# Optimization experiments

Hardware: AMD Instinct MI355X
Metric: run time of the kernel (lower is better)

## Reference

```python
import jax, jax.numpy as jnp
import numpy as np

EMBED_DIM = 1024
HID = EMBED_DIM // 2
N = 32768
L2_REG = 0.001
BN_EPS = 1e-5


def setup_inputs() -> dict:
    key = jax.random.key(0)
    ks = jax.random.split(key, 8)
    inp = {
        "item_emb": jax.random.normal(ks[0], (N, EMBED_DIM), jnp.float32),
        "pos_item_emb": jax.random.normal(ks[1], (N, EMBED_DIM), jnp.float32),
        "neg_item_emb": jax.random.normal(ks[2], (N, EMBED_DIM), jnp.float32),
        # Linear 1: embed_dim -> embed_dim/2 (xavier_normal init, zero bias)
        "W1": jax.random.normal(ks[3], (HID, EMBED_DIM), jnp.float32) * np.sqrt(2.0 / (EMBED_DIM + HID)),
        "b1": jnp.zeros((HID,), jnp.float32),
        # BatchNorm1d params / running stats (eval-mode semantics)
        "gamma": jnp.ones((HID,), jnp.float32),
        "beta": jnp.zeros((HID,), jnp.float32),
        "run_mean": jnp.zeros((HID,), jnp.float32),
        "run_var": jnp.ones((HID,), jnp.float32),
        # Linear 2: embed_dim/2 -> embed_dim
        "W2": jax.random.normal(ks[4], (EMBED_DIM, HID), jnp.float32) * np.sqrt(2.0 / (EMBED_DIM + HID)),
        "b2": jnp.zeros((EMBED_DIM,), jnp.float32),
    }
    return inp


def _net(x, W1, b1, gamma, beta, run_mean, run_var, W2, b2):
    # Linear -> BatchNorm1d (eval stats) -> LeakyReLU(0.1) -> (Dropout=identity) -> Linear
    h = x @ W1.T + b1                                   # [N, HID]
    h = (h - run_mean) * jax.lax.rsqrt(run_var + BN_EPS) * gamma + beta
    h = jnp.where(h >= 0, h, 0.1 * h)
    return h @ W2.T + b2                                # [N, EMBED_DIM]


def reference(item_emb, pos_item_emb, neg_item_emb,
              W1, b1, gamma, beta, run_mean, run_var, W2, b2):
    net = lambda x: _net(x, W1, b1, gamma, beta, run_mean, run_var, W2, b2)
    anchor_e = net(item_emb)
    pos_e = net(pos_item_emb)
    neg_e = net(neg_item_emb)

    dist_pos = jnp.linalg.norm(anchor_e - pos_e, axis=1)  # [N]
    dist_neg = jnp.linalg.norm(anchor_e - neg_e, axis=1)  # [N]

    # fused replacement of the per-sample python loop
    margins = jnp.where(dist_neg < dist_pos, dist_pos - dist_neg, 0.0)
    margin = jnp.quantile(margins, 0.25)  # Q1, linear interpolation (matches torch)

    loss_triplet = jax.nn.relu(dist_neg ** 2 - dist_pos ** 2 + margin)
    l2 = L2_REG * (jnp.sum(anchor_e ** 2) + jnp.sum(pos_e ** 2) + jnp.sum(neg_e ** 2)) / anchor_e.shape[0]
    return jnp.mean(loss_triplet + l2)
```

## Files before the change

### kernel.cpp

```cpp
#include <hip/hip_runtime.h>

#define NROWS 32768
#define DIM   1024
#define HIDD  512
#define M3    (3*NROWS)

using bf16x8 = __attribute__((ext_vector_type(8))) short;
using f32x4  = __attribute__((ext_vector_type(4))) float;

#define MFMA16(a,b,c) __builtin_amdgcn_mfma_f32_16x16x32_bf16(a,b,c,0,0,0)
#define WAIT_VM(N)  asm volatile("s_waitcnt vmcnt(" #N ")" ::: "memory")
#define WAIT_LGKM0  asm volatile("s_waitcnt lgkmcnt(0)" ::: "memory")
#define MEMFENCE    asm volatile("" ::: "memory")
#define BAR()       __builtin_amdgcn_s_barrier()
#define SCHEDB()    __builtin_amdgcn_sched_barrier(0)
#define SP1()       __builtin_amdgcn_s_setprio(1)
#define SP0()       __builtin_amdgcn_s_setprio(0)

static __device__ __forceinline__ unsigned short f2bf(float f) {
    unsigned u = __float_as_uint(f);
    u += 0x7FFFu + ((u >> 16) & 1u);
    return (unsigned short)(u >> 16);
}
static __device__ __forceinline__ unsigned cvtpk(float a, float b) {
    unsigned r;
    asm("v_cvt_pk_bf16_f32 %0, %1, %2" : "=v"(r) : "v"(a), "v"(b));
    return r;
}
static __device__ __forceinline__ void gload16(const void* gsrc, void* ldst) {
    __builtin_amdgcn_global_load_lds(
        (const __attribute__((address_space(1))) unsigned int*)gsrc,
        (__attribute__((address_space(3))) unsigned int*)ldst,
        16, 0, 0);
}

__global__ __launch_bounds__(256)
void cvt2_kernel(const float* __restrict__ src1, unsigned short* __restrict__ dst1,
                 const float* __restrict__ src2, unsigned short* __restrict__ dst2,
                 int n4each)
{
    const int i = blockIdx.x * 256 + threadIdx.x;
    const float* src = (i < n4each) ? src1 : src2;
    unsigned short* dst = (i < n4each) ? dst1 : dst2;
    const int j = (i < n4each) ? i : (i - n4each);
    if (j < n4each) {
        float4 v = reinterpret_cast<const float4*>(src)[j];
        uint2 o;
        o.x = cvtpk(v.x, v.y);
        o.y = cvtpk(v.z, v.w);
        reinterpret_cast<uint2*>(dst)[j] = o;
    }
}

__global__ __launch_bounds__(512)
void gemm1_mfma(const float* __restrict__ x0, const float* __restrict__ x1,
                const float* __restrict__ x2,
                const unsigned short* __restrict__ W1bf,
                const float* __restrict__ b1, const float* __restrict__ gamma,
                const float* __restrict__ beta, const float* __restrict__ rmean,
                const float* __restrict__ rvar,
                unsigned short* __restrict__ h)
{
    __shared__ unsigned short Abuf[128*64];
    __shared__ unsigned short Bbuf[2*128*32];

    const int lin = blockIdx.x;
    const int wgid = (lin & 7) * 384 + (lin >> 3);
    const int cb = wgid & 3;
    const int rb = wgid >> 2;
    const int tid  = threadIdx.x;
    const int lane = tid & 63, w = tid >> 6;
    const int wr = w >> 2, wc = w & 3;
    const int row0 = rb * 128;
    const int s = row0 >> 15;
    const float* x = (s == 0) ? x0 : (s == 1 ? x1 : x2);
    const int rl0 = row0 & (NROWS - 1);
    const int col0 = cb * 128;
    const int l15 = lane & 15, lq = lane >> 4;

    f32x4 acc[4][2] = {};
    float4 aR[4];

    #pragma unroll
    for (int p = 0; p < 4; ++p) {
        const int f = p * 512 + tid;
        const int r = f >> 4, c4 = f & 15;
        aR[p] = *reinterpret_cast<const float4*>(&x[(size_t)(rl0 + r) * DIM + c4 * 4]);
    }

    for (int t = 0; t < 16; ++t) {
        const int k0 = t * 64;
        #pragma unroll
        for (int p = 0; p < 4; ++p) {
            const int f = p * 512 + tid;
            const int r = f >> 4, c4 = f & 15;
            const unsigned off = (unsigned)((r * 128 + c4 * 8) ^ ((r & 7) << 4));
            uint2 o;
            o.x = cvtpk(aR[p].x, aR[p].y);
            o.y = cvtpk(aR[p].z, aR[p].w);
            *reinterpret_cast<uint2*>(reinterpret_cast<char*>(Abuf) + off) = o;
        }
        #pragma unroll
        for (int c = 0; c < 2; ++c) {
            const int f = c * 512 + tid;
            const int panel = f >> 9;
            const int cc = (f >> 2) & 127;
            const int chunk = (f & 3) ^ ((cc >> 1) & 3);
            gload16(&W1bf[(size_t)(col0 + cc) * DIM + k0 + panel * 32 + chunk * 8],
                    reinterpret_cast<char*>(Bbuf) + (size_t)f * 16);
        }
        __syncthreads();
        if (t < 15) {
            #pragma unroll
            for (int p = 0; p < 4; ++p) {
                const int f = p * 512 + tid;
                const int r = f >> 4, c4 = f & 15;
                aR[p] = *reinterpret_cast<const float4*>(
                    &x[(size_t)(rl0 + r) * DIM + k0 + 64 + c4 * 4]);
            }
        }
        bf16x8 bfv[2][2];
        #pragma unroll
        for (int kk = 0; kk < 2; ++kk)
            #pragma unroll
            for (int n = 0; n < 2; ++n) {
                const int colr = wc*32 + n*16 + l15;
                const int slq = lq ^ ((colr >> 1) & 3);
                bfv[kk][n] = *reinterpret_cast<const bf16x8*>(
                    reinterpret_cast<char*>(Bbuf) + kk*8192 + colr*64 + slq*16);
            }
        #pragma unroll
        for (int kk = 0; kk < 2; ++kk)
            #pragma unroll
            for (int m = 0; m < 4; ++m) {
                const int row = wr*64 + m*16 + l15;
                const unsigned ab = (unsigned)((row*128 + kk*64 + lq*16) ^ ((row & 7) << 4));
                bf16x8 af = *reinterpret_cast<const bf16x8*>(
                    reinterpret_cast<char*>(Abuf) + ab);
                #pragma unroll
                for (int n = 0; n < 2; ++n)
                    acc[m][n] = MFMA16(af, bfv[kk][n], acc[m][n]);
            }
        __syncthreads();
    }

    float As[2], Bsc[2];
    #pragma unroll
    for (int n = 0; n < 2; ++n) {
        const int c = col0 + wc*32 + n*16 + l15;
        const float inv = rsqrtf(rvar[c] + 1e-5f);
        As[n]  = inv * gamma[c];
        Bsc[n] = (b1[c] - rmean[c]) * As[n] + beta[c];
    }
    #pragma unroll
    for (int m = 0; m < 4; ++m) {
        const int rbase = row0 + wr*64 + m*16 + lq*4;
        #pragma unroll
        for (int n = 0; n < 2; ++n) {
            const int c = col0 + wc*32 + n*16 + l15;
            #pragma unroll
            for (int i = 0; i < 4; ++i) {
                float v = fmaf(acc[m][n][i], As[n], Bsc[n]);
                v = (v >= 0.f) ? v : 0.1f * v;
                h[(size_t)(rbase + i) * HIDD + c] = f2bf(v);
            }
        }
    }
}

__global__ __launch_bounds__(512, 1)
void gemm2_mfma(const unsigned short* __restrict__ h,
                const unsigned short* __restrict__ W2bf,
                const float* __restrict__ b2,
                float* __restrict__ pdp, float* __restrict__ pdn,
                float* __restrict__ pl2)
{
    __shared__ char smem[114688];
    char* const Ab = smem;
    char* const Bb = smem + 49152;

    const int lin = blockIdx.x;
    const int wgid = (lin & 7) * 256 + (lin >> 3);
    const int cb = wgid & 3;
    const int rb = wgid >> 2;
    const int tid  = threadIdx.x;
    const int lane = tid & 63, w = tid >> 6;
    const int wm = w >> 2, wn = w & 3;
    const int row0 = rb * 64;
    const int col0 = cb * 256;
    const int l15 = lane & 15, lq = lane >> 4;

    f32x4 acc[6][4] = {};

    auto issueA = [&](int k0, char* Adst) {
        #pragma unroll
        for (int i = 0; i < 3; ++i) {
            const int f = i * 512 + tid;
            const int mrow = f >> 3, c = f & 7;
            const int mf = mrow >> 4, rr = mrow & 15;
            const int ss = mf % 3, rf = mf / 3;
            gload16(&h[((size_t)ss * NROWS + row0 + rf * 16 + rr) * HIDD + k0 + ((c ^ (mrow & 7)) << 3)],
                    Adst + f * 16);
        }
    };
    auto issueB = [&](int k0, char* Bdst) {
        #pragma unroll
        for (int i = 0; i < 4; ++i) {
            const int f = i * 512 + tid;
            const int col = f >> 3, c = f & 7;
            gload16(&W2bf[(size_t)(col0 + col) * HIDD + k0 + ((c ^ (col & 7)) << 3)],
                    Bdst + f * 16);
        }
    };
    auto readA = [&](bf16x8 (&a)[3][2], int mh, char* Abase) {
        #pragma unroll
        for (int mm = 0; mm < 3; ++mm) {
            const int row = (wm * 6 + mh * 3 + mm) * 16 + l15;
            const int swz = (row & 7) << 4;
            #pragma unroll
            for (int ks = 0; ks < 2; ++ks)
                a[mm][ks] = *reinterpret_cast<const bf16x8*>(
                    Abase + ((row * 128 + ks * 64 + lq * 16) ^ swz));
        }
    };
    auto readB = [&](bf16x8 (&b)[2][2], int nh, char* Bbase) {
        #pragma unroll
        for (int nn = 0; nn < 2; ++nn) {
            const int col = wn * 64 + (nh * 2 + nn) * 16 + l15;
            const int swz = (col & 7) << 4;
            #pragma unroll
            for (int ks = 0; ks < 2; ++ks)
                b[nn][ks] = *reinterpret_cast<const bf16x8*>(
                    Bbase + ((col * 128 + ks * 64 + lq * 16) ^ swz));
        }
    };

    issueA(0, Ab);
    MEMFENCE;
    issueB(0, Bb);
    WAIT_VM(0);
    BAR();

    for (int t = 0; t < 8; ++t) {
        char* const Apt = Ab + (t & 1) * 24576;
        char* const Apn = Ab + ((t & 1) ^ 1) * 24576;
        char* const Bpt = Bb + (t & 1) * 32768;
        char* const Bpn = Bb + ((t & 1) ^ 1) * 32768;
        const int kn = ((t < 7) ? (t + 1) : 7) * 64;

        bf16x8 a[3][2], b[2][2], a2[3][2];
        readA(a, 0, Apt);
        readB(b, 0, Bpt);
        issueA(kn, Apn);
        MEMFENCE;
        issueB(kn, Bpn);
        BAR(); WAIT_LGKM0; SCHEDB(); SP1();
        #pragma unroll
        for (int mm = 0; mm < 3; ++mm)
            #pragma unroll
            for (int nn = 0; nn < 2; ++nn)
                #pragma unroll
                for (int ks = 0; ks < 2; ++ks)
                    acc[mm][nn] = MFMA16(a[mm][ks], b[nn][ks], acc[mm][nn]);
        SP0(); BAR();
        readB(b, 1, Bpt);
        BAR(); WAIT_LGKM0; SCHEDB(); SP1();
        #pragma unroll
        for (int mm = 0; mm < 3; ++mm)
            #pragma unroll
            for (int nn = 0; nn < 2; ++nn)
                #pragma unroll
                for (int ks = 0; ks < 2; ++ks)
                    acc[mm][2 + nn] = MFMA16(a[mm][ks], b[nn][ks], acc[mm][2 + nn]);
        SP0(); BAR();
        readA(a2, 1, Apt);
        BAR(); WAIT_LGKM0; SCHEDB(); SP1();
        #pragma unroll
        for (int mm = 0; mm < 3; ++mm)
            #pragma unroll
            for (int nn = 0; nn < 2; ++nn)
                #pragma unroll
                for (int ks = 0; ks < 2; ++ks)
                    acc[3 + mm][2 + nn] = MFMA16(a2[mm][ks], b[nn][ks], acc[3 + mm][2 + nn]);
        SP0(); BAR();
        readB(b, 0, Bpt);
        WAIT_VM(0);
        BAR(); WAIT_LGKM0; SCHEDB(); SP1();
        #pragma unroll
        for (int mm = 0; mm < 3; ++mm)
            #pragma unroll
            for (int nn = 0; nn < 2; ++nn)
                #pragma unroll
                for (int ks = 0; ks < 2; ++ks)
                    acc[3 + mm][nn] = MFMA16(a2[mm][ks], b[nn][ks], acc[3 + mm][nn]);
        SP0(); BAR();
    }

    float b2c[4];
    #pragma unroll
    for (int nf = 0; nf < 4; ++nf) b2c[nf] = b2[col0 + wn * 64 + nf * 16 + l15];
    float l2t = 0.f;
    #pragma unroll
    for (int mh = 0; mh < 2; ++mh) {
        const int rbase = row0 + (wm * 2 + mh) * 16 + lq * 4;
        #pragma unroll
        for (int i = 0; i < 4; ++i) {
            float dp = 0.f, dn = 0.f;
            #pragma unroll
            for (int nf = 0; nf < 4; ++nf) {
                const float ea = acc[mh * 3 + 0][nf][i] + b2c[nf];
                const float ep = acc[mh * 3 + 1][nf][i] + b2c[nf];
                const float en = acc[mh * 3 + 2][nf][i] + b2c[nf];
                dp += (ea - ep) * (ea - ep);
                dn += (ea - en) * (ea - en);
                l2t += ea * ea + ep * ep + en * en;
            }
            #pragma unroll
            for (int mm = 1; mm < 16; mm <<= 1) {
                dp += __shfl_xor(dp, mm);
                dn += __shfl_xor(dn, mm);
            }
            if (l15 == 0) {
                pdp[(size_t)(cb * 4 + wn) * NROWS + rbase + i] = dp;
                pdn[(size_t)(cb * 4 + wn) * NROWS + rbase + i] = dn;
            }
        }
    }
    #pragma unroll
    for (int mm = 1; mm < 64; mm <<= 1) l2t += __shfl_xor(l2t, mm);
    __syncthreads();
    float* const l2red = (float*)smem;
    if (lane == 0) l2red[w] = l2t;
    __syncthreads();
    if (tid == 0) {
        float t = 0.f;
        #pragma unroll
        for (int ww = 0; ww < 8; ++ww) t += l2red[ww];
        pl2[wgid] = t;
    }
}

__global__ __launch_bounds__(256)
void margins_kernel(const float* __restrict__ pdp, const float* __restrict__ pdn,
                    float* __restrict__ margins, float* __restrict__ dd)
{
    const int r = blockIdx.x * 256 + threadIdx.x;
    float dp2 = 0.f, dn2 = 0.f;
    #pragma unroll
    for (int q = 0; q < 16; ++q) {
        dp2 += pdp[(size_t)q * NROWS + r];
        dn2 += pdn[(size_t)q * NROWS + r];
    }
    dd[r] = dn2 - dp2;
    margins[r] = (dn2 < dp2) ? (sqrtf(dp2) - sqrtf(dn2)) : 0.f;
}

__global__ __launch_bounds__(1024)
void final_kernel(const float* __restrict__ pl2, int npl2,
                  const float* __restrict__ margins, const float* __restrict__ dd,
                  float* __restrict__ out)
{
    __shared__ unsigned hist[256];
    __shared__ float warp_red[16];
    __shared__ unsigned wsum[4];
    __shared__ unsigned sh_prefix;
    __shared__ int sh_k;
    __shared__ float sh_l2;
    __shared__ unsigned sh_cle;
    __shared__ unsigned sh_minAbove;
    const int tid = threadIdx.x;

    float l2 = 0.f;
    for (int i = tid; i < npl2; i += 1024) l2 += pl2[i];
    #pragma unroll
    for (int m = 1; m < 64; m <<= 1) l2 += __shfl_xor(l2, m);
    if ((tid & 63) == 0) warp_red[tid >> 6] = l2;
    __syncthreads();
    if (tid == 0) {
        float t = 0.f;
        for (int w = 0; w < 16; ++w) t += warp_red[w];
        sh_l2 = t;
        sh_k = 8191; sh_prefix = 0u;
        sh_cle = 0u; sh_minAbove = 0xFFFFFFFFu;
    }
    __syncthreads();

    for (int shift = 24; shift >= 0; shift -= 8) {
        if (tid < 256) hist[tid] = 0u;
        __syncthreads();
        const unsigned prefix = sh_prefix;
        const int kcur = sh_k;
        const unsigned mask = (shift == 24) ? 0u : (0xFFFFFFFFu << (shift + 8));
        for (int i = tid; i < NROWS; i += 1024) {
            const unsigned key = __float_as_uint(margins[i]);
            if (((key ^ prefix) & mask) == 0u)
                atomicAdd(&hist[(key >> shift) & 255u], 1u);
        }
        __syncthreads();
        unsigned v = 0, cme = 0;
        if (tid < 256) {
            cme = hist[tid];
            v = cme;
            #pragma unroll
            for (int off = 1; off < 64; off <<= 1) {
                unsigned tt = __shfl_up(v, off);
                if ((tid & 63) >= off) v += tt;
            }
            if ((tid & 63) == 63) wsum[tid >> 6] = v;
        }
        __syncthreads();
        if (tid < 256) {
            unsigned wo = 0;
            for (int i = 0; i < (tid >> 6); ++i) wo += wsum[i];
            const unsigned incl = v + wo;
            const unsigned excl = incl - cme;
            if ((unsigned)kcur >= excl && (unsigned)kcur < incl) {
                sh_prefix = prefix | ((unsigned)tid << shift);
                sh_k = kcur - (int)excl;
            }
        }
        __syncthreads();
    }
    const unsigned p1u = sh_prefix;

    unsigned lc = 0, lmin = 0xFFFFFFFFu;
    for (int i = tid; i < NROWS; i += 1024) {
        const unsigned key = __float_as_uint(margins[i]);
        if (key <= p1u) ++lc; else lmin = min(lmin, key);
    }
    #pragma unroll
    for (int m = 1; m < 64; m <<= 1) {
        lc += __shfl_xor(lc, m);
        lmin = min(lmin, (unsigned)__shfl_xor((int)lmin, m));
    }
    if ((tid & 63) == 0) {
        atomicAdd(&sh_cle, lc);
        atomicMin(&sh_minAbove, lmin);
    }
    __syncthreads();
    const float p1 = __uint_as_float(p1u);
    const float p2 = (sh_cle >= 8193u) ? p1 : __uint_as_float(sh_minAbove);
    const float margin = p1 + 0.75f * (p2 - p1);

    float ssum = 0.f;
    for (int i = tid; i < NROWS; i += 1024) {
        const float t = dd[i] + margin;
        ssum += (t > 0.f) ? t : 0.f;
    }
    #pragma unroll
    for (int m = 1; m < 64; m <<= 1) ssum += __shfl_xor(ssum, m);
    if ((tid & 63) == 0) warp_red[tid >> 6] = ssum;
    __syncthreads();
    if (tid == 0) {
        float S = 0.f;
        for (int w = 0; w < 16; ++w) S += warp_red[w];
        out[0] = S / (float)NROWS + 1e-3f * sh_l2 / (float)NROWS;
    }
}

extern "C" void kernel_launch(void* const* d_in, const int* in_sizes, int n_in,
                              void* d_out, int out_size, void* d_ws, size_t ws_size,
                              hipStream_t stream) {
    (void)in_sizes; (void)n_in; (void)out_size; (void)ws_size;
    const float* item = (const float*)d_in[0];
    const float* pos  = (const float*)d_in[1];
    const float* neg  = (const float*)d_in[2];
    const float* W1   = (const float*)d_in[3];
    const float* b1   = (const float*)d_in[4];
    const float* gam  = (const float*)d_in[5];
    const float* bet  = (const float*)d_in[6];
    const float* rmu  = (const float*)d_in[7];
    const float* rvr  = (const float*)d_in[8];
    const float* W2   = (const float*)d_in[9];
    const float* b2   = (const float*)d_in[10];

    char* ws = (char*)d_ws;
    unsigned short* h = (unsigned short*)ws;
    size_t off = (size_t)M3 * HIDD * sizeof(unsigned short);
    unsigned short* W1bf = (unsigned short*)(ws + off); off += (size_t)HIDD * DIM * 2;
    unsigned short* W2bf = (unsigned short*)(ws + off); off += (size_t)DIM * HIDD * 2;
    float* pdp = (float*)(ws + off); off += (size_t)16 * NROWS * 4;
    float* pdn = (float*)(ws + off); off += (size_t)16 * NROWS * 4;
    float* pl2 = (float*)(ws + off); off += (size_t)2048 * 4;
    float* margins = (float*)(ws + off); off += (size_t)NROWS * 4;
    float* dd = (float*)(ws + off); off += (size_t)NROWS * 4;

    const int n4each = HIDD * DIM / 4;
    cvt2_kernel<<<dim3(2 * n4each / 256), 256, 0, stream>>>(W1, W1bf, W2, W2bf, n4each);
    gemm1_mfma<<<dim3(3072), 512, 0, stream>>>(
        item, pos, neg, W1bf, b1, gam, bet, rmu, rvr, h);
    gemm2_mfma<<<dim3(2048), 512, 0, stream>>>(
        h, W2bf, b2, pdp, pdn, pl2);
    margins_kernel<<<dim3(NROWS/256), 256, 0, stream>>>(pdp, pdn, margins, dd);
    final_kernel<<<1, 1024, 0, stream>>>(pl2, 2048, margins, dd, (float*)d_out);
}
```

Measured before the change: 409.2 us.

## Halve gemm2 column tile to fit two workgroups per CU

The gemm2 column tile shrinks from 256 to 128, which halves the B shared-memory buffers and the accumulator registers. This allows launch_bounds of 2 workgroups per CU and doubles the grid to 4096 blocks. The partial distance buffers grow from 16 to 32 slices, and margins_kernel and final_kernel are updated to match. In exchange, each A tile (the h rows) is loaded twice as often, so global traffic rises and each block does less MFMA work per load.

```diff
diff --git a/kernel.cpp b/kernel.cpp
--- a/kernel.cpp
+++ b/kernel.cpp
@@ -168,29 +168,29 @@
     }
 }
 
-__global__ __launch_bounds__(512, 1)
+__global__ __launch_bounds__(512, 2)
 void gemm2_mfma(const unsigned short* __restrict__ h,
                 const unsigned short* __restrict__ W2bf,
                 const float* __restrict__ b2,
                 float* __restrict__ pdp, float* __restrict__ pdn,
                 float* __restrict__ pl2)
 {
-    __shared__ char smem[114688];
+    __shared__ char smem[81920];
     char* const Ab = smem;
     char* const Bb = smem + 49152;
 
     const int lin = blockIdx.x;
-    const int wgid = (lin & 7) * 256 + (lin >> 3);
-    const int cb = wgid & 3;
-    const int rb = wgid >> 2;
+    const int wgid = (lin & 7) * 512 + (lin >> 3);
+    const int cb = wgid & 7;
+    const int rb = wgid >> 3;
     const int tid  = threadIdx.x;
     const int lane = tid & 63, w = tid >> 6;
     const int wm = w >> 2, wn = w & 3;
     const int row0 = rb * 64;
-    const int col0 = cb * 256;
+    const int col0 = cb * 128;
     const int l15 = lane & 15, lq = lane >> 4;
 
-    f32x4 acc[6][4] = {};
+    f32x4 acc[6][2] = {};
 
     auto issueA = [&](int k0, char* Adst) {
         #pragma unroll
@@ -205,7 +205,7 @@
     };
     auto issueB = [&](int k0, char* Bdst) {
         #pragma unroll
-        for (int i = 0; i < 4; ++i) {
+        for (int i = 0; i < 2; ++i) {
             const int f = i * 512 + tid;
             const int col = f >> 3, c = f & 7;
             gload16(&W2bf[(size_t)(col0 + col) * HIDD + k0 + ((c ^ (col & 7)) << 3)],
@@ -223,16 +223,13 @@
                     Abase + ((row * 128 + ks * 64 + lq * 16) ^ swz));
         }
     };
-    auto readB = [&](bf16x8 (&b)[2][2], int nh, char* Bbase) {
-        #pragma unroll
-        for (int nn = 0; nn < 2; ++nn) {
-            const int col = wn * 64 + (nh * 2 + nn) * 16 + l15;
-            const int swz = (col & 7) << 4;
-            #pragma unroll
-            for (int ks = 0; ks < 2; ++ks)
-                b[nn][ks] = *reinterpret_cast<const bf16x8*>(
-                    Bbase + ((col * 128 + ks * 64 + lq * 16) ^ swz));
-        }
+    auto readB = [&](bf16x8 (&b)[2], int nh, char* Bbase) {
+        const int col = wn * 32 + nh * 16 + l15;
+        const int swz = (col & 7) << 4;
+        #pragma unroll
+        for (int ks = 0; ks < 2; ++ks)
+            b[ks] = *reinterpret_cast<const bf16x8*>(
+                Bbase + ((col * 128 + ks * 64 + lq * 16) ^ swz));
     };
 
     issueA(0, Ab);
@@ -244,11 +241,11 @@
     for (int t = 0; t < 8; ++t) {
         char* const Apt = Ab + (t & 1) * 24576;
         char* const Apn = Ab + ((t & 1) ^ 1) * 24576;
-        char* const Bpt = Bb + (t & 1) * 32768;
-        char* const Bpn = Bb + ((t & 1) ^ 1) * 32768;
+        char* const Bpt = Bb + (t & 1) * 16384;
+        char* const Bpn = Bb + ((t & 1) ^ 1) * 16384;
         const int kn = ((t < 7) ? (t + 1) : 7) * 64;
 
-        bf16x8 a[3][2], b[2][2], a2[3][2];
+        bf16x8 a[3][2], b[2], a2[3][2];
         readA(a, 0, Apt);
         readB(b, 0, Bpt);
         issueA(kn, Apn);
@@ -258,30 +255,24 @@
         #pragma unroll
         for (int mm = 0; mm < 3; ++mm)
             #pragma unroll
-            for (int nn = 0; nn < 2; ++nn)
-                #pragma unroll
-                for (int ks = 0; ks < 2; ++ks)
-                    acc[mm][nn] = MFMA16(a[mm][ks], b[nn][ks], acc[mm][nn]);
+            for (int ks = 0; ks < 2; ++ks)
+                acc[mm][0] = MFMA16(a[mm][ks], b[ks], acc[mm][0]);
         SP0(); BAR();
         readB(b, 1, Bpt);
         BAR(); WAIT_LGKM0; SCHEDB(); SP1();
         #pragma unroll
         for (int mm = 0; mm < 3; ++mm)
             #pragma unroll
-            for (int nn = 0; nn < 2; ++nn)
-                #pragma unroll
-                for (int ks = 0; ks < 2; ++ks)
-                    acc[mm][2 + nn] = MFMA16(a[mm][ks], b[nn][ks], acc[mm][2 + nn]);
+            for (int ks = 0; ks < 2; ++ks)
+                acc[mm][1] = MFMA16(a[mm][ks], b[ks], acc[mm][1]);
         SP0(); BAR();
         readA(a2, 1, Apt);
         BAR(); WAIT_LGKM0; SCHEDB(); SP1();
         #pragma unroll
         for (int mm = 0; mm < 3; ++mm)
             #pragma unroll
-            for (int nn = 0; nn < 2; ++nn)
-                #pragma unroll
-                for (int ks = 0; ks < 2; ++ks)
-                    acc[3 + mm][2 + nn] = MFMA16(a2[mm][ks], b[nn][ks], acc[3 + mm][2 + nn]);
+            for (int ks = 0; ks < 2; ++ks)
+                acc[3 + mm][1] = MFMA16(a2[mm][ks], b[ks], acc[3 + mm][1]);
         SP0(); BAR();
         readB(b, 0, Bpt);
         WAIT_VM(0);
@@ -289,16 +280,14 @@
         #pragma unroll
         for (int mm = 0; mm < 3; ++mm)
             #pragma unroll
-            for (int nn = 0; nn < 2; ++nn)
-                #pragma unroll
-                for (int ks = 0; ks < 2; ++ks)
-                    acc[3 + mm][nn] = MFMA16(a2[mm][ks], b[nn][ks], acc[3 + mm][nn]);
+            for (int ks = 0; ks < 2; ++ks)
+                acc[3 + mm][0] = MFMA16(a2[mm][ks], b[ks], acc[3 + mm][0]);
         SP0(); BAR();
     }
 
-    float b2c[4];
-    #pragma unroll
-    for (int nf = 0; nf < 4; ++nf) b2c[nf] = b2[col0 + wn * 64 + nf * 16 + l15];
+    float b2c[2];
+    b2c[0] = b2[col0 + wn * 32 + l15];
+    b2c[1] = b2[col0 + wn * 32 + 16 + l15];
     float l2t = 0.f;
     #pragma unroll
     for (int mh = 0; mh < 2; ++mh) {
@@ -307,7 +296,7 @@
         for (int i = 0; i < 4; ++i) {
             float dp = 0.f, dn = 0.f;
             #pragma unroll
-            for (int nf = 0; nf < 4; ++nf) {
+            for (int nf = 0; nf < 2; ++nf) {
                 const float ea = acc[mh * 3 + 0][nf][i] + b2c[nf];
                 const float ep = acc[mh * 3 + 1][nf][i] + b2c[nf];
                 const float en = acc[mh * 3 + 2][nf][i] + b2c[nf];
@@ -347,7 +336,7 @@
     const int r = blockIdx.x * 256 + threadIdx.x;
     float dp2 = 0.f, dn2 = 0.f;
     #pragma unroll
-    for (int q = 0; q < 16; ++q) {
+    for (int q = 0; q < 32; ++q) {
         dp2 += pdp[(size_t)q * NROWS + r];
         dn2 += pdn[(size_t)q * NROWS + r];
     }
@@ -479,9 +468,9 @@
     size_t off = (size_t)M3 * HIDD * sizeof(unsigned short);
     unsigned short* W1bf = (unsigned short*)(ws + off); off += (size_t)HIDD * DIM * 2;
     unsigned short* W2bf = (unsigned short*)(ws + off); off += (size_t)DIM * HIDD * 2;
-    float* pdp = (float*)(ws + off); off += (size_t)16 * NROWS * 4;
-    float* pdn = (float*)(ws + off); off += (size_t)16 * NROWS * 4;
-    float* pl2 = (float*)(ws + off); off += (size_t)2048 * 4;
+    float* pdp = (float*)(ws + off); off += (size_t)32 * NROWS * 4;
+    float* pdn = (float*)(ws + off); off += (size_t)32 * NROWS * 4;
+    float* pl2 = (float*)(ws + off); off += (size_t)4096 * 4;
     float* margins = (float*)(ws + off); off += (size_t)NROWS * 4;
     float* dd = (float*)(ws + off); off += (size_t)NROWS * 4;
 
@@ -489,8 +478,8 @@
     cvt2_kernel<<<dim3(2 * n4each / 256), 256, 0, stream>>>(W1, W1bf, W2, W2bf, n4each);
     gemm1_mfma<<<dim3(3072), 512, 0, stream>>>(
         item, pos, neg, W1bf, b1, gam, bet, rmu, rvr, h);
-    gemm2_mfma<<<dim3(2048), 512, 0, stream>>>(
+    gemm2_mfma<<<dim3(4096), 512, 0, stream>>>(
         h, W2bf, b2, pdp, pdn, pl2);
     margins_kernel<<<dim3(NROWS/256), 256, 0, stream>>>(pdp, pdn, margins, dd);
-    final_kernel<<<1, 1024, 0, stream>>>(pl2, 2048, margins, dd, (float*)d_out);
-}
+    final_kernel<<<1, 1024, 0, stream>>>(pl2, 4096, margins, dd, (float*)d_out);
+}
```

Result: slower. 462.4 us (+13.0%).
